# Kernel tuning notes

Measured on AMD Instinct MI355X. Metric: run time of the kernel, lower is better.

## Reference

```python
import jax, jax.numpy as jnp
import numpy as np

DIM_M = 512
NEG_INF = -1e30


def setup_inputs() -> dict:
    key = jax.random.key(0)
    k1, k2, k3, k4, k5, k6, k7 = jax.random.split(key, 7)
    B, Lc, Lq, d = 16, 1024, 512, DIM_M
    C = jax.random.normal(k1, (B, Lc, d), dtype=jnp.float32)
    Q = jax.random.normal(k2, (B, Lq, d), dtype=jnp.float32)
    cmask = jax.random.randint(k3, (B, Lc), 0, 2).astype(jnp.float32)
    qmask = jax.random.randint(k4, (B, Lq), 0, 2).astype(jnp.float32)
    lim = np.sqrt(1.0 / d)
    w = jax.random.uniform(k5, (3 * d,), minval=-lim, maxval=lim, dtype=jnp.float32)
    # out_linear: Linear(4d -> d), torch default init
    bound = np.sqrt(1.0 / (4 * d))
    out_w = jax.random.uniform(k6, (d, 4 * d), minval=-bound, maxval=bound, dtype=jnp.float32)
    out_b = jax.random.uniform(k7, (d,), minval=-bound, maxval=bound, dtype=jnp.float32)
    return {"C": C, "Q": Q, "cmask": cmask, "qmask": qmask, "w": w, "out_w": out_w, "out_b": out_b}


def _mask_logits(t, m):
    return t * m + (1.0 - m) * NEG_INF


def reference(C, Q, cmask, qmask, w, out_w, out_b):
    d = C.shape[-1]
    w1, w2, w3 = w[:d], w[d:2 * d], w[2 * d:]
    # Decomposed trilinear similarity (same math as cat([Ct,Qt,Ct*Qt]) @ w):
    # S[b,i,j] = C[b,i]@w1 + Q[b,j]@w2 + (C[b,i]*w3) @ Q[b,j]
    S = (C @ w1)[:, :, None] + (Q @ w2)[:, None, :] \
        + jnp.einsum('bid,bjd->bij', C * w3, Q)  # [B, Lc, Lq]
    qm = qmask[:, None, :]  # [B, 1, Lq]
    cm = cmask[:, :, None]  # [B, Lc, 1]
    S1 = jax.nn.softmax(_mask_logits(S, qm), axis=2)  # over Lq
    S2 = jax.nn.softmax(_mask_logits(S, cm), axis=1)  # over Lc
    A = jnp.einsum('bij,bjd->bid', S1, Q)  # [B, Lc, d]
    # bmm(bmm(S1, S2^T), C) == S1 @ (S2^T @ C) by associativity (cheaper)
    S2TC = jnp.einsum('bij,bid->bjd', S2, C)  # [B, Lq, d]
    Bm = jnp.einsum('bij,bjd->bid', S1, S2TC)  # [B, Lc, d]
    out = jnp.concatenate([C, A, C * A, C * Bm], axis=2)  # [B, Lc, 4d]
    # dropout inactive (inference); out_linear
    return out @ out_w.T + out_b
```

## Files before the change

### kernel.cpp

```cpp
#include <hip/hip_runtime.h>
#include <hip/hip_bf16.h>


#define NB 16
#define LC 1024
#define LQ 512
#define DM 512
#define D4 2048
#define NEGINF (-1e30f)
#define BK 32
#define LDAp 40

typedef __bf16 v8bf __attribute__((ext_vector_type(8)));
typedef __bf16 v4bf __attribute__((ext_vector_type(4)));
typedef float  v4f  __attribute__((ext_vector_type(4)));

#define MFMA16 __builtin_amdgcn_mfma_f32_16x16x32_bf16

#define TILE_SETUP \
  const int t = threadIdx.x, lane = t & 63, wave = t >> 6; \
  const int wm = wave >> 1, wn = wave & 1, quad = lane >> 4, col = lane & 15;

#define ZERO_ACC \
  v4f acc[4][4]; \
  _Pragma("unroll") for (int x = 0; x < 4; ++x) \
  _Pragma("unroll") for (int y = 0; y < 4; ++y) \
  _Pragma("unroll") for (int r = 0; r < 4; ++r) acc[x][y][r] = 0.f;

#define FRAG_MMA(AL, BL) do { \
  v8bf af_[4], bf_[4]; \
  _Pragma("unroll") for (int x = 0; x < 4; ++x) \
    af_[x] = *(const v8bf*)&AL[(wm * 64 + x * 16 + col) * LDAp + quad * 8]; \
  _Pragma("unroll") for (int y = 0; y < 4; ++y) \
    bf_[y] = *(const v8bf*)&BL[(wn * 64 + y * 16 + col) * LDAp + quad * 8]; \
  _Pragma("unroll") for (int x = 0; x < 4; ++x) \
  _Pragma("unroll") for (int y = 0; y < 4; ++y) \
    acc[x][y] = MFMA16(af_[x], bf_[y], acc[x][y], 0, 0, 0); \
} while (0)

__device__ __forceinline__ void xcd_remap(int& bx, int& by, int& bz) {
  const int gx = gridDim.x, gy = gridDim.y, gz = gridDim.z;
  int flat = bx + gx * (by + gy * bz);
  int per = (gx * gy * gz) >> 3;
  int nw = (flat & 7) * per + (flat >> 3);
  bx = nw % gx;
  int r = nw / gx;
  by = r % gy;
  bz = r / gy;
}

__global__ void k_rowdots(const float* __restrict__ C, const float* __restrict__ Q,
                          const float* __restrict__ w,
                          float* __restrict__ cw1, float* __restrict__ qw2) {
  const int wid = threadIdx.x >> 6, lane = threadIdx.x & 63;
  const int row = blockIdx.x * 4 + wid;
  const bool isC = row < NB * LC;
  const float* src = isC ? (C + (size_t)row * DM) : (Q + (size_t)(row - NB * LC) * DM);
  const float* wv  = isC ? w : (w + DM);
  float v = 0.f;
#pragma unroll
  for (int tt = 0; tt < 8; ++tt) {
    int k = lane + 64 * tt;
    v += src[k] * wv[k];
  }
#pragma unroll
  for (int off = 32; off; off >>= 1) v += __shfl_down(v, off, 64);
  if (lane == 0) {
    if (isC) cw1[row] = v;
    else     qw2[row - NB * LC] = v;
  }
}

__global__ __launch_bounds__(256) void k_mfma_S(
    const float* __restrict__ C, const float* __restrict__ Q, const float* __restrict__ w,
    const float* __restrict__ cw1, const float* __restrict__ qw2, float* __restrict__ S) {
  __shared__ __bf16 Al[128 * LDAp], Bl[128 * LDAp];
  int bx = blockIdx.x, by = blockIdx.y, bz = blockIdx.z;
  xcd_remap(bx, by, bz);
  const int b = bz, i0 = by * 128, j0 = bx * 128;
  TILE_SETUP
  const float* Cb = C + (size_t)b * LC * DM;
  const float* Qb = Q + (size_t)b * LQ * DM;
  const float* w3 = w + 2 * DM;
  const int sr = t >> 1, skc = (t & 1) * 16;
  ZERO_ACC
  for (int k0 = 0; k0 < DM; k0 += BK) {
    const float* ca = Cb + (size_t)(i0 + sr) * DM + k0 + skc;
    const float* qa = Qb + (size_t)(j0 + sr) * DM + k0 + skc;
    const float* wa = w3 + k0 + skc;
#pragma unroll
    for (int u = 0; u < 4; ++u) {
      float4 cf = *(const float4*)(ca + 4 * u);
      float4 wf = *(const float4*)(wa + 4 * u);
      float4 qf = *(const float4*)(qa + 4 * u);
      v4bf ah, bh;
      ah[0] = (__bf16)(cf.x * wf.x); ah[1] = (__bf16)(cf.y * wf.y);
      ah[2] = (__bf16)(cf.z * wf.z); ah[3] = (__bf16)(cf.w * wf.w);
      bh[0] = (__bf16)qf.x; bh[1] = (__bf16)qf.y; bh[2] = (__bf16)qf.z; bh[3] = (__bf16)qf.w;
      *(v4bf*)&Al[sr * LDAp + skc + 4 * u] = ah;
      *(v4bf*)&Bl[sr * LDAp + skc + 4 * u] = bh;
    }
    __syncthreads();
    FRAG_MMA(Al, Bl);
    __syncthreads();
  }
  float* Sb = S + (size_t)b * LC * LQ;
#pragma unroll
  for (int x = 0; x < 4; ++x) {
    const int mB = i0 + wm * 64 + x * 16 + quad * 4;
    float cv[4];
#pragma unroll
    for (int r = 0; r < 4; ++r) cv[r] = cw1[b * LC + mB + r];
#pragma unroll
    for (int y = 0; y < 4; ++y) {
      const int j = j0 + wn * 64 + y * 16 + col;
      const float qv = qw2[b * LQ + j];
#pragma unroll
      for (int r = 0; r < 4; ++r)
        Sb[(size_t)(mB + r) * LQ + j] = acc[x][y][r] + cv[r] + qv;
    }
  }
}

__global__ __launch_bounds__(1024) void k_softstat(
    const float* __restrict__ S, const float* __restrict__ qmask,
    const float* __restrict__ cmask, __bf16* __restrict__ S1,
    float2* __restrict__ pstat) {
  __shared__ float2 cst[16][LQ];
  const int b = blockIdx.y, ic = blockIdx.x;
  const int tid = threadIdx.x, wv = tid >> 6, lane = tid & 63;
  const float* qm  = qmask + b * LQ;
  const float* cm  = cmask + b * LC + ic * 64;
  const float* Sb  = S  + ((size_t)b * LC + ic * 64) * LQ;
  __bf16*      S1b = S1 + ((size_t)b * LC + ic * 64) * LQ;
  float colm[8], cols[8];
#pragma unroll
  for (int tt = 0; tt < 8; ++tt) { colm[tt] = -3e38f; cols[tt] = 0.f; }
  for (int it = 0; it < 4; ++it) {
    const int r = wv * 4 + it;
    const float cmv = cm[r];
    const float* Srow = Sb + (size_t)r * LQ;
    float sv[8], l1[8];
    float m = -3e38f;
#pragma unroll
    for (int tt = 0; tt < 8; ++tt) {
      int j = lane + 64 * tt;
      sv[tt] = Srow[j];
      float qv = qm[j];
      l1[tt] = qv * sv[tt] + (1.f - qv) * NEGINF;
      m = fmaxf(m, l1[tt]);
    }
#pragma unroll
    for (int off = 32; off; off >>= 1) m = fmaxf(m, __shfl_xor(m, off, 64));
    float e[8], s = 0.f;
#pragma unroll
    for (int tt = 0; tt < 8; ++tt) { e[tt] = __expf(l1[tt] - m); s += e[tt]; }
#pragma unroll
    for (int off = 32; off; off >>= 1) s += __shfl_xor(s, off, 64);
    const float inv = 1.f / s;
#pragma unroll
    for (int tt = 0; tt < 8; ++tt)
      S1b[(size_t)r * LQ + lane + 64 * tt] = (__bf16)(e[tt] * inv);
#pragma unroll
    for (int tt = 0; tt < 8; ++tt) {
      float l2 = cmv * sv[tt] + (1.f - cmv) * NEGINF;
      if (l2 > colm[tt]) { cols[tt] *= __expf(colm[tt] - l2); colm[tt] = l2; }
      cols[tt] += __expf(l2 - colm[tt]);
    }
  }
#pragma unroll
  for (int tt = 0; tt < 8; ++tt) cst[wv][lane + 64 * tt] = make_float2(colm[tt], cols[tt]);
  __syncthreads();
  if (tid < LQ) {
    float M = -3e38f, Sd = 0.f;
#pragma unroll
    for (int k = 0; k < 16; ++k) {
      float2 p = cst[k][tid];
      float nM = fmaxf(M, p.x);
      Sd = Sd * __expf(M - nM) + p.y * __expf(p.x - nM);
      M = nM;
    }
    pstat[((size_t)(b * 16 + ic) * LQ) + tid] = make_float2(M, Sd);
  }
}

__global__ void k_colwrite(const float* __restrict__ S, const float* __restrict__ cmask,
                           const float2* __restrict__ pstat, __bf16* __restrict__ S2) {
  __shared__ float Mf[64], If[64];
  const int b = blockIdx.z, ic = blockIdx.y, j0 = blockIdx.x * 64;
  const int c = threadIdx.x & 63, ip = threadIdx.x >> 6;
  if (threadIdx.x < 64) {
    float M = -3e38f, Sd = 0.f;
#pragma unroll
    for (int k = 0; k < 16; ++k) {
      float2 p = pstat[((size_t)(b * 16 + k) * LQ) + j0 + threadIdx.x];
      float nM = fmaxf(M, p.x);
      Sd = Sd * __expf(M - nM) + p.y * __expf(p.x - nM);
      M = nM;
    }
    Mf[threadIdx.x] = M; If[threadIdx.x] = 1.f / Sd;
  }
  __syncthreads();
  const float M = Mf[c], inv = If[c];
  const float* Sb = S + ((size_t)b * LC + ic * 64) * LQ;
  const float* cm = cmask + b * LC + ic * 64;
  __bf16* S2b = S2 + ((size_t)b * LC + ic * 64) * LQ;
  for (int r = ip; r < 64; r += 4) {
    float mk = cm[r];
    float logit = mk * Sb[(size_t)r * LQ + j0 + c] + (1.f - mk) * NEGINF;
    S2b[(size_t)r * LQ + j0 + c] = (__bf16)(__expf(logit - M) * inv);
  }
}

__global__ __launch_bounds__(256) void k_mfma_A(
    const __bf16* __restrict__ S1, const float* __restrict__ Q, __bf16* __restrict__ Aw) {
  __shared__ __bf16 Al[128 * LDAp], Bl[128 * LDAp];
  int bx = blockIdx.x, by = blockIdx.y, bz = blockIdx.z;
  xcd_remap(bx, by, bz);
  const int b = bz, i0 = by * 128, n0 = bx * 128;
  TILE_SETUP
  const __bf16* S1b = S1 + (size_t)b * LC * LQ;
  const float*  Qb  = Q  + (size_t)b * LQ * DM;
  const int ar = t >> 1, akc = (t & 1) * 16;
  const int kk = t >> 3, nn = (t & 7) * 16;
  ZERO_ACC
  for (int k0 = 0; k0 < LQ; k0 += BK) {
    const __bf16* sa = S1b + (size_t)(i0 + ar) * LQ + k0 + akc;
#pragma unroll
    for (int u = 0; u < 2; ++u)
      *(v8bf*)&Al[ar * LDAp + akc + 8 * u] = *(const v8bf*)(sa + 8 * u);
    const float* qa = Qb + (size_t)(k0 + kk) * DM + n0 + nn;
#pragma unroll
    for (int u = 0; u < 4; ++u) {
      float4 f = *(const float4*)(qa + 4 * u);
      Bl[(nn + 4 * u + 0) * LDAp + kk] = (__bf16)f.x;
      Bl[(nn + 4 * u + 1) * LDAp + kk] = (__bf16)f.y;
      Bl[(nn + 4 * u + 2) * LDAp + kk] = (__bf16)f.z;
      Bl[(nn + 4 * u + 3) * LDAp + kk] = (__bf16)f.w;
    }
    __syncthreads();
    FRAG_MMA(Al, Bl);
    __syncthreads();
  }
  __bf16* Ab = Aw + (size_t)b * LC * DM;
#pragma unroll
  for (int x = 0; x < 4; ++x) {
    const int mB = i0 + wm * 64 + x * 16 + quad * 4;
#pragma unroll
    for (int y = 0; y < 4; ++y) {
      const int n = n0 + wn * 64 + y * 16 + col;
#pragma unroll
      for (int r = 0; r < 4; ++r)
        Ab[(size_t)(mB + r) * DM + n] = (__bf16)acc[x][y][r];
    }
  }
}

__global__ __launch_bounds__(256) void k_mfma_T(
    const __bf16* __restrict__ S2, const float* __restrict__ C, __bf16* __restrict__ S2TCT) {
  __shared__ __bf16 Al[128 * LDAp], Bl[128 * LDAp];
  int bx = blockIdx.x, by = blockIdx.y, bz = blockIdx.z;
  xcd_remap(bx, by, bz);
  const int b = bz, j0 = by * 128, n0 = bx * 128;
  TILE_SETUP
  const __bf16* S2b = S2 + (size_t)b * LC * LQ;
  const float*  Cb  = C  + (size_t)b * LC * DM;
  const int kk = t >> 3, jj = (t & 7) * 16;
  ZERO_ACC
  for (int k0 = 0; k0 < LC; k0 += BK) {
    const __bf16* sa = S2b + (size_t)(k0 + kk) * LQ + j0 + jj;
    v8bf s0 = *(const v8bf*)(sa), s1 = *(const v8bf*)(sa + 8);
#pragma unroll
    for (int u = 0; u < 8; ++u) {
      Al[(jj + u) * LDAp + kk]     = s0[u];
      Al[(jj + 8 + u) * LDAp + kk] = s1[u];
    }
    const float* cb2 = Cb + (size_t)(k0 + kk) * DM + n0 + jj;
#pragma unroll
    for (int u = 0; u < 4; ++u) {
      float4 f = *(const float4*)(cb2 + 4 * u);
      Bl[(jj + 4 * u + 0) * LDAp + kk] = (__bf16)f.x;
      Bl[(jj + 4 * u + 1) * LDAp + kk] = (__bf16)f.y;
      Bl[(jj + 4 * u + 2) * LDAp + kk] = (__bf16)f.z;
      Bl[(jj + 4 * u + 3) * LDAp + kk] = (__bf16)f.w;
    }
    __syncthreads();
    FRAG_MMA(Al, Bl);
    __syncthreads();
  }
#pragma unroll
  for (int x = 0; x < 4; ++x) {
    const int jB = j0 + wm * 64 + x * 16 + quad * 4;
#pragma unroll
    for (int y = 0; y < 4; ++y) {
      const int n = n0 + wn * 64 + y * 16 + col;
      v4bf h;
#pragma unroll
      for (int r = 0; r < 4; ++r) h[r] = (__bf16)acc[x][y][r];
      *(v4bf*)&S2TCT[((size_t)b * DM + n) * LQ + jB] = h;
    }
  }
}

__global__ __launch_bounds__(256) void k_mfma_Bm(
    const __bf16* __restrict__ S1, const __bf16* __restrict__ S2TCT, __bf16* __restrict__ Bmw) {
  __shared__ __bf16 Al[128 * LDAp], Bl[128 * LDAp];
  int bx = blockIdx.x, by = blockIdx.y, bz = blockIdx.z;
  xcd_remap(bx, by, bz);
  const int b = bz, i0 = by * 128, n0 = bx * 128;
  TILE_SETUP
  const __bf16* S1b = S1 + (size_t)b * LC * LQ;
  const __bf16* Tb  = S2TCT + (size_t)b * DM * LQ;
  const int ar = t >> 1, akc = (t & 1) * 16;
  ZERO_ACC
  for (int k0 = 0; k0 < LQ; k0 += BK) {
    const __bf16* sa = S1b + (size_t)(i0 + ar) * LQ + k0 + akc;
    const __bf16* ta = Tb + (size_t)(n0 + ar) * LQ + k0 + akc;
#pragma unroll
    for (int u = 0; u < 2; ++u) {
      *(v8bf*)&Al[ar * LDAp + akc + 8 * u] = *(const v8bf*)(sa + 8 * u);
      *(v8bf*)&Bl[ar * LDAp + akc + 8 * u] = *(const v8bf*)(ta + 8 * u);
    }
    __syncthreads();
    FRAG_MMA(Al, Bl);
    __syncthreads();
  }
  __bf16* Bb = Bmw + (size_t)b * LC * DM;
#pragma unroll
  for (int x = 0; x < 4; ++x) {
    const int mB = i0 + wm * 64 + x * 16 + quad * 4;
#pragma unroll
    for (int y = 0; y < 4; ++y) {
      const int n = n0 + wn * 64 + y * 16 + col;
#pragma unroll
      for (int r = 0; r < 4; ++r)
        Bb[(size_t)(mB + r) * DM + n] = (__bf16)acc[x][y][r];
    }
  }
}

__global__ __launch_bounds__(256) void k_mfma_out(
    const float* __restrict__ C, const __bf16* __restrict__ Aw, const __bf16* __restrict__ Bmw,
    const float* __restrict__ OW, const float* __restrict__ ob, float* __restrict__ out) {
  __shared__ __bf16 Asg[4][128 * LDAp], Bsg[4][128 * LDAp];
  int bx = blockIdx.x, by = blockIdx.y, bz = blockIdx.z;
  xcd_remap(bx, by, bz);
  const int b = bz, i0 = by * 128, n0 = bx * 128;
  TILE_SETUP
  const float*  Cb = C   + (size_t)b * LC * DM;
  const __bf16* Ab = Aw  + (size_t)b * LC * DM;
  const __bf16* Bb = Bmw + (size_t)b * LC * DM;
  const int sr = t >> 1, skc = (t & 1) * 16;
  ZERO_ACC
  for (int kl0 = 0; kl0 < DM; kl0 += BK) {
    const float*  cr = Cb + (size_t)(i0 + sr) * DM + kl0 + skc;
    const __bf16* ap = Ab + (size_t)(i0 + sr) * DM + kl0 + skc;
    const __bf16* bp = Bb + (size_t)(i0 + sr) * DM + kl0 + skc;
#pragma unroll
    for (int u = 0; u < 2; ++u) {
      float4 f0 = *(const float4*)(cr + 8 * u);
      float4 f1 = *(const float4*)(cr + 8 * u + 4);
      v8bf av = *(const v8bf*)(ap + 8 * u);
      v8bf bv = *(const v8bf*)(bp + 8 * u);
      float cf[8] = {f0.x, f0.y, f0.z, f0.w, f1.x, f1.y, f1.z, f1.w};
      v8bf hC, hCA, hCB;
#pragma unroll
      for (int e = 0; e < 8; ++e) {
        hC[e]  = (__bf16)cf[e];
        hCA[e] = (__bf16)(cf[e] * (float)av[e]);
        hCB[e] = (__bf16)(cf[e] * (float)bv[e]);
      }
      const int off = sr * LDAp + skc + 8 * u;
      *(v8bf*)&Asg[0][off] = hC;
      *(v8bf*)&Asg[1][off] = av;
      *(v8bf*)&Asg[2][off] = hCA;
      *(v8bf*)&Asg[3][off] = hCB;
    }
    const float* owr = OW + (size_t)(n0 + sr) * D4 + kl0 + skc;
#pragma unroll
    for (int s = 0; s < 4; ++s) {
#pragma unroll
      for (int u = 0; u < 4; ++u) {
        float4 f = *(const float4*)(owr + s * DM + 4 * u);
        v4bf h; h[0] = (__bf16)f.x; h[1] = (__bf16)f.y; h[2] = (__bf16)f.z; h[3] = (__bf16)f.w;
        *(v4bf*)&Bsg[s][sr * LDAp + skc + 4 * u] = h;
      }
    }
    __syncthreads();
#pragma unroll
    for (int s = 0; s < 4; ++s) FRAG_MMA(Asg[s], Bsg[s]);
    __syncthreads();
  }
  float* outb = out + (size_t)b * LC * DM;
#pragma unroll
  for (int x = 0; x < 4; ++x) {
    const int mB = i0 + wm * 64 + x * 16 + quad * 4;
#pragma unroll
    for (int y = 0; y < 4; ++y) {
      const int n = n0 + wn * 64 + y * 16 + col;
      const float bv = ob[n];
#pragma unroll
      for (int r = 0; r < 4; ++r)
        outb[(size_t)(mB + r) * DM + n] = acc[x][y][r] + bv;
    }
  }
}

extern "C" void kernel_launch(void* const* d_in, const int* in_sizes, int n_in,
                              void* d_out, int out_size, void* d_ws, size_t ws_size,
                              hipStream_t stream) {
  const float* C     = (const float*)d_in[0];
  const float* Q     = (const float*)d_in[1];
  const float* cmask = (const float*)d_in[2];
  const float* qmask = (const float*)d_in[3];
  const float* w     = (const float*)d_in[4];
  const float* out_w = (const float*)d_in[5];
  const float* out_b = (const float*)d_in[6];
  float* out = (float*)d_out;

  char* base = (char*)d_ws;
  float*  cw1   = (float*)base;
  float*  qw2   = (float*)(base + 65536);
  char*   R     = base + 131072;
  float*  S     = (float*)R;
  __bf16* Aw    = (__bf16*)R;
  __bf16* Bmw   = (__bf16*)(R + (16u << 20));
  __bf16* S1    = (__bf16*)(base + 131072 + (32u << 20));
  __bf16* S2    = (__bf16*)(base + 131072 + (48u << 20));
  __bf16* S2TCT = (__bf16*)(base + 131072 + (64u << 20));
  float2* pstat = (float2*)S2TCT;
  (void)in_sizes; (void)n_in; (void)out_size; (void)ws_size;

  k_rowdots<<<(NB * LC + NB * LQ) / 4, 256, 0, stream>>>(C, Q, w, cw1, qw2);
  k_mfma_S<<<dim3(LQ / 128, LC / 128, NB), 256, 0, stream>>>(C, Q, w, cw1, qw2, S);
  k_softstat<<<dim3(LC / 64, NB), 1024, 0, stream>>>(S, qmask, cmask, S1, pstat);
  k_colwrite<<<dim3(LQ / 64, LC / 64, NB), 256, 0, stream>>>(S, cmask, pstat, S2);
  k_mfma_A<<<dim3(DM / 128, LC / 128, NB), 256, 0, stream>>>(S1, Q, Aw);
  k_mfma_T<<<dim3(DM / 128, LQ / 128, NB), 256, 0, stream>>>(S2, C, S2TCT);
  k_mfma_Bm<<<dim3(DM / 128, LC / 128, NB), 256, 0, stream>>>(S1, S2TCT, Bmw);
  k_mfma_out<<<dim3(DM / 128, LC / 128, NB), 256, 0, stream>>>(C, Aw, Bmw, out_w, out_b, out);
}
```

Baseline: 319.3 us.

## Pre-transpose Q, C and S2 to bf16 and use 8-wave GEMM tiles

Adds a transpose kernel that writes bf16 transposed copies of Q and C, and makes the column-softmax kernel emit S2 transposed through an LDS tile. With these layouts the A and T GEMMs can fill LDS with contiguous vector loads instead of scattered scalar transposed stores. All MFMA kernels move to 512-thread blocks, 8 waves with a 64x32 tile per wave, and the output GEMM runs in two passes over half-size LDS buffers. The cost is two extra transpose launches and more workspace traffic, with buffers aliased in the workspace.

```diff
diff --git a/kernel.cpp b/kernel.cpp
--- a/kernel.cpp
+++ b/kernel.cpp
@@ -17,24 +17,25 @@
 
 #define MFMA16 __builtin_amdgcn_mfma_f32_16x16x32_bf16
 
-#define TILE_SETUP \
+#define TILE_SETUP8 \
   const int t = threadIdx.x, lane = t & 63, wave = t >> 6; \
-  const int wm = wave >> 1, wn = wave & 1, quad = lane >> 4, col = lane & 15;
-
-#define ZERO_ACC \
-  v4f acc[4][4]; \
+  const int wm = wave >> 2, wn = wave & 3, quad = lane >> 4, col = lane & 15; \
+  const int sr = t >> 2, skc = (t & 3) * 8;
+
+#define ZERO_ACC8 \
+  v4f acc[4][2]; \
   _Pragma("unroll") for (int x = 0; x < 4; ++x) \
-  _Pragma("unroll") for (int y = 0; y < 4; ++y) \
+  _Pragma("unroll") for (int y = 0; y < 2; ++y) \
   _Pragma("unroll") for (int r = 0; r < 4; ++r) acc[x][y][r] = 0.f;
 
-#define FRAG_MMA(AL, BL) do { \
-  v8bf af_[4], bf_[4]; \
+#define FRAG_MMA8(AL, BL) do { \
+  v8bf af_[4], bf_[2]; \
   _Pragma("unroll") for (int x = 0; x < 4; ++x) \
     af_[x] = *(const v8bf*)&AL[(wm * 64 + x * 16 + col) * LDAp + quad * 8]; \
-  _Pragma("unroll") for (int y = 0; y < 4; ++y) \
-    bf_[y] = *(const v8bf*)&BL[(wn * 64 + y * 16 + col) * LDAp + quad * 8]; \
+  _Pragma("unroll") for (int y = 0; y < 2; ++y) \
+    bf_[y] = *(const v8bf*)&BL[(wn * 32 + y * 16 + col) * LDAp + quad * 8]; \
   _Pragma("unroll") for (int x = 0; x < 4; ++x) \
-  _Pragma("unroll") for (int y = 0; y < 4; ++y) \
+  _Pragma("unroll") for (int y = 0; y < 2; ++y) \
     acc[x][y] = MFMA16(af_[x], bf_[y], acc[x][y], 0, 0, 0); \
 } while (0)
 
@@ -49,6 +50,14 @@
   bz = r / gy;
 }
 
+__device__ __forceinline__ v8bf cvt8(const float* p) {
+  float4 f0 = *(const float4*)p, f1 = *(const float4*)(p + 4);
+  v8bf h;
+  h[0] = (__bf16)f0.x; h[1] = (__bf16)f0.y; h[2] = (__bf16)f0.z; h[3] = (__bf16)f0.w;
+  h[4] = (__bf16)f1.x; h[5] = (__bf16)f1.y; h[6] = (__bf16)f1.z; h[7] = (__bf16)f1.w;
+  return h;
+}
+
 __global__ void k_rowdots(const float* __restrict__ C, const float* __restrict__ Q,
                           const float* __restrict__ w,
                           float* __restrict__ cw1, float* __restrict__ qw2) {
@@ -71,37 +80,48 @@
   }
 }
 
-__global__ __launch_bounds__(256) void k_mfma_S(
+__global__ void k_transpose(const float* __restrict__ in, __bf16* __restrict__ outT,
+                            int R, int Cd) {
+  __shared__ __bf16 tile[64][66];
+  const int b = blockIdx.z;
+  const int r0 = blockIdx.y * 64, c0 = blockIdx.x * 64;
+  const int tr = threadIdx.x >> 6, tc = threadIdx.x & 63;
+  const float* inb = in + (size_t)b * R * Cd;
+  __bf16* outb = outT + (size_t)b * Cd * R;
+  for (int r = tr; r < 64; r += 4)
+    tile[r][tc] = (__bf16)inb[(size_t)(r0 + r) * Cd + c0 + tc];
+  __syncthreads();
+  for (int c = tr; c < 64; c += 4)
+    outb[(size_t)(c0 + c) * R + r0 + tc] = tile[tc][c];
+}
+
+__global__ __launch_bounds__(512) void k_mfma_S(
     const float* __restrict__ C, const float* __restrict__ Q, const float* __restrict__ w,
     const float* __restrict__ cw1, const float* __restrict__ qw2, float* __restrict__ S) {
   __shared__ __bf16 Al[128 * LDAp], Bl[128 * LDAp];
   int bx = blockIdx.x, by = blockIdx.y, bz = blockIdx.z;
   xcd_remap(bx, by, bz);
   const int b = bz, i0 = by * 128, j0 = bx * 128;
-  TILE_SETUP
+  TILE_SETUP8
   const float* Cb = C + (size_t)b * LC * DM;
   const float* Qb = Q + (size_t)b * LQ * DM;
   const float* w3 = w + 2 * DM;
-  const int sr = t >> 1, skc = (t & 1) * 16;
-  ZERO_ACC
+  ZERO_ACC8
   for (int k0 = 0; k0 < DM; k0 += BK) {
     const float* ca = Cb + (size_t)(i0 + sr) * DM + k0 + skc;
     const float* qa = Qb + (size_t)(j0 + sr) * DM + k0 + skc;
     const float* wa = w3 + k0 + skc;
-#pragma unroll
-    for (int u = 0; u < 4; ++u) {
-      float4 cf = *(const float4*)(ca + 4 * u);
-      float4 wf = *(const float4*)(wa + 4 * u);
-      float4 qf = *(const float4*)(qa + 4 * u);
-      v4bf ah, bh;
-      ah[0] = (__bf16)(cf.x * wf.x); ah[1] = (__bf16)(cf.y * wf.y);
-      ah[2] = (__bf16)(cf.z * wf.z); ah[3] = (__bf16)(cf.w * wf.w);
-      bh[0] = (__bf16)qf.x; bh[1] = (__bf16)qf.y; bh[2] = (__bf16)qf.z; bh[3] = (__bf16)qf.w;
-      *(v4bf*)&Al[sr * LDAp + skc + 4 * u] = ah;
-      *(v4bf*)&Bl[sr * LDAp + skc + 4 * u] = bh;
-    }
-    __syncthreads();
-    FRAG_MMA(Al, Bl);
+    float4 c0 = *(const float4*)ca, c1 = *(const float4*)(ca + 4);
+    float4 w0 = *(const float4*)wa, w1 = *(const float4*)(wa + 4);
+    v8bf ah;
+    ah[0] = (__bf16)(c0.x * w0.x); ah[1] = (__bf16)(c0.y * w0.y);
+    ah[2] = (__bf16)(c0.z * w0.z); ah[3] = (__bf16)(c0.w * w0.w);
+    ah[4] = (__bf16)(c1.x * w1.x); ah[5] = (__bf16)(c1.y * w1.y);
+    ah[6] = (__bf16)(c1.z * w1.z); ah[7] = (__bf16)(c1.w * w1.w);
+    *(v8bf*)&Al[sr * LDAp + skc] = ah;
+    *(v8bf*)&Bl[sr * LDAp + skc] = cvt8(qa);
+    __syncthreads();
+    FRAG_MMA8(Al, Bl);
     __syncthreads();
   }
   float* Sb = S + (size_t)b * LC * LQ;
@@ -112,8 +132,8 @@
 #pragma unroll
     for (int r = 0; r < 4; ++r) cv[r] = cw1[b * LC + mB + r];
 #pragma unroll
-    for (int y = 0; y < 4; ++y) {
-      const int j = j0 + wn * 64 + y * 16 + col;
+    for (int y = 0; y < 2; ++y) {
+      const int j = j0 + wn * 32 + y * 16 + col;
       const float qv = qw2[b * LQ + j];
 #pragma unroll
       for (int r = 0; r < 4; ++r)
@@ -185,8 +205,9 @@
 }
 
 __global__ void k_colwrite(const float* __restrict__ S, const float* __restrict__ cmask,
-                           const float2* __restrict__ pstat, __bf16* __restrict__ S2) {
+                           const float2* __restrict__ pstat, __bf16* __restrict__ S2T) {
   __shared__ float Mf[64], If[64];
+  __shared__ __bf16 tile[64][66];
   const int b = blockIdx.z, ic = blockIdx.y, j0 = blockIdx.x * 64;
   const int c = threadIdx.x & 63, ip = threadIdx.x >> 6;
   if (threadIdx.x < 64) {
@@ -204,42 +225,32 @@
   const float M = Mf[c], inv = If[c];
   const float* Sb = S + ((size_t)b * LC + ic * 64) * LQ;
   const float* cm = cmask + b * LC + ic * 64;
-  __bf16* S2b = S2 + ((size_t)b * LC + ic * 64) * LQ;
   for (int r = ip; r < 64; r += 4) {
     float mk = cm[r];
     float logit = mk * Sb[(size_t)r * LQ + j0 + c] + (1.f - mk) * NEGINF;
-    S2b[(size_t)r * LQ + j0 + c] = (__bf16)(__expf(logit - M) * inv);
-  }
-}
-
-__global__ __launch_bounds__(256) void k_mfma_A(
-    const __bf16* __restrict__ S1, const float* __restrict__ Q, __bf16* __restrict__ Aw) {
+    tile[r][c] = (__bf16)(__expf(logit - M) * inv);
+  }
+  __syncthreads();
+  __bf16* S2Tb = S2T + ((size_t)b * LQ + j0) * LC + ic * 64;
+  for (int jr = ip; jr < 64; jr += 4)
+    S2Tb[(size_t)jr * LC + c] = tile[c][jr];
+}
+
+__global__ __launch_bounds__(512) void k_mfma_A(
+    const __bf16* __restrict__ S1, const __bf16* __restrict__ QT, __bf16* __restrict__ Aw) {
   __shared__ __bf16 Al[128 * LDAp], Bl[128 * LDAp];
   int bx = blockIdx.x, by = blockIdx.y, bz = blockIdx.z;
   xcd_remap(bx, by, bz);
   const int b = bz, i0 = by * 128, n0 = bx * 128;
-  TILE_SETUP
+  TILE_SETUP8
   const __bf16* S1b = S1 + (size_t)b * LC * LQ;
-  const float*  Qb  = Q  + (size_t)b * LQ * DM;
-  const int ar = t >> 1, akc = (t & 1) * 16;
-  const int kk = t >> 3, nn = (t & 7) * 16;
-  ZERO_ACC
+  const __bf16* QTb = QT + (size_t)b * DM * LQ;
+  ZERO_ACC8
   for (int k0 = 0; k0 < LQ; k0 += BK) {
-    const __bf16* sa = S1b + (size_t)(i0 + ar) * LQ + k0 + akc;
-#pragma unroll
-    for (int u = 0; u < 2; ++u)
-      *(v8bf*)&Al[ar * LDAp + akc + 8 * u] = *(const v8bf*)(sa + 8 * u);
-    const float* qa = Qb + (size_t)(k0 + kk) * DM + n0 + nn;
-#pragma unroll
-    for (int u = 0; u < 4; ++u) {
-      float4 f = *(const float4*)(qa + 4 * u);
-      Bl[(nn + 4 * u + 0) * LDAp + kk] = (__bf16)f.x;
-      Bl[(nn + 4 * u + 1) * LDAp + kk] = (__bf16)f.y;
-      Bl[(nn + 4 * u + 2) * LDAp + kk] = (__bf16)f.z;
-      Bl[(nn + 4 * u + 3) * LDAp + kk] = (__bf16)f.w;
-    }
-    __syncthreads();
-    FRAG_MMA(Al, Bl);
+    *(v8bf*)&Al[sr * LDAp + skc] = *(const v8bf*)(S1b + (size_t)(i0 + sr) * LQ + k0 + skc);
+    *(v8bf*)&Bl[sr * LDAp + skc] = *(const v8bf*)(QTb + (size_t)(n0 + sr) * LQ + k0 + skc);
+    __syncthreads();
+    FRAG_MMA8(Al, Bl);
     __syncthreads();
   }
   __bf16* Ab = Aw + (size_t)b * LC * DM;
@@ -247,8 +258,8 @@
   for (int x = 0; x < 4; ++x) {
     const int mB = i0 + wm * 64 + x * 16 + quad * 4;
 #pragma unroll
-    for (int y = 0; y < 4; ++y) {
-      const int n = n0 + wn * 64 + y * 16 + col;
+    for (int y = 0; y < 2; ++y) {
+      const int n = n0 + wn * 32 + y * 16 + col;
 #pragma unroll
       for (int r = 0; r < 4; ++r)
         Ab[(size_t)(mB + r) * DM + n] = (__bf16)acc[x][y][r];
@@ -256,44 +267,29 @@
   }
 }
 
-__global__ __launch_bounds__(256) void k_mfma_T(
-    const __bf16* __restrict__ S2, const float* __restrict__ C, __bf16* __restrict__ S2TCT) {
+__global__ __launch_bounds__(512) void k_mfma_T(
+    const __bf16* __restrict__ S2T, const __bf16* __restrict__ CT, __bf16* __restrict__ S2TCT) {
   __shared__ __bf16 Al[128 * LDAp], Bl[128 * LDAp];
   int bx = blockIdx.x, by = blockIdx.y, bz = blockIdx.z;
   xcd_remap(bx, by, bz);
   const int b = bz, j0 = by * 128, n0 = bx * 128;
-  TILE_SETUP
-  const __bf16* S2b = S2 + (size_t)b * LC * LQ;
-  const float*  Cb  = C  + (size_t)b * LC * DM;
-  const int kk = t >> 3, jj = (t & 7) * 16;
-  ZERO_ACC
+  TILE_SETUP8
+  const __bf16* S2Tb = S2T + (size_t)b * LQ * LC;
+  const __bf16* CTb  = CT  + (size_t)b * DM * LC;
+  ZERO_ACC8
   for (int k0 = 0; k0 < LC; k0 += BK) {
-    const __bf16* sa = S2b + (size_t)(k0 + kk) * LQ + j0 + jj;
-    v8bf s0 = *(const v8bf*)(sa), s1 = *(const v8bf*)(sa + 8);
-#pragma unroll
-    for (int u = 0; u < 8; ++u) {
-      Al[(jj + u) * LDAp + kk]     = s0[u];
-      Al[(jj + 8 + u) * LDAp + kk] = s1[u];
-    }
-    const float* cb2 = Cb + (size_t)(k0 + kk) * DM + n0 + jj;
-#pragma unroll
-    for (int u = 0; u < 4; ++u) {
-      float4 f = *(const float4*)(cb2 + 4 * u);
-      Bl[(jj + 4 * u + 0) * LDAp + kk] = (__bf16)f.x;
-      Bl[(jj + 4 * u + 1) * LDAp + kk] = (__bf16)f.y;
-      Bl[(jj + 4 * u + 2) * LDAp + kk] = (__bf16)f.z;
-      Bl[(jj + 4 * u + 3) * LDAp + kk] = (__bf16)f.w;
-    }
-    __syncthreads();
-    FRAG_MMA(Al, Bl);
+    *(v8bf*)&Al[sr * LDAp + skc] = *(const v8bf*)(S2Tb + (size_t)(j0 + sr) * LC + k0 + skc);
+    *(v8bf*)&Bl[sr * LDAp + skc] = *(const v8bf*)(CTb  + (size_t)(n0 + sr) * LC + k0 + skc);
+    __syncthreads();
+    FRAG_MMA8(Al, Bl);
     __syncthreads();
   }
 #pragma unroll
   for (int x = 0; x < 4; ++x) {
     const int jB = j0 + wm * 64 + x * 16 + quad * 4;
 #pragma unroll
-    for (int y = 0; y < 4; ++y) {
-      const int n = n0 + wn * 64 + y * 16 + col;
+    for (int y = 0; y < 2; ++y) {
+      const int n = n0 + wn * 32 + y * 16 + col;
       v4bf h;
 #pragma unroll
       for (int r = 0; r < 4; ++r) h[r] = (__bf16)acc[x][y][r];
@@ -302,27 +298,21 @@
   }
 }
 
-__global__ __launch_bounds__(256) void k_mfma_Bm(
+__global__ __launch_bounds__(512) void k_mfma_Bm(
     const __bf16* __restrict__ S1, const __bf16* __restrict__ S2TCT, __bf16* __restrict__ Bmw) {
   __shared__ __bf16 Al[128 * LDAp], Bl[128 * LDAp];
   int bx = blockIdx.x, by = blockIdx.y, bz = blockIdx.z;
   xcd_remap(bx, by, bz);
   const int b = bz, i0 = by * 128, n0 = bx * 128;
-  TILE_SETUP
+  TILE_SETUP8
   const __bf16* S1b = S1 + (size_t)b * LC * LQ;
   const __bf16* Tb  = S2TCT + (size_t)b * DM * LQ;
-  const int ar = t >> 1, akc = (t & 1) * 16;
-  ZERO_ACC
+  ZERO_ACC8
   for (int k0 = 0; k0 < LQ; k0 += BK) {
-    const __bf16* sa = S1b + (size_t)(i0 + ar) * LQ + k0 + akc;
-    const __bf16* ta = Tb + (size_t)(n0 + ar) * LQ + k0 + akc;
-#pragma unroll
-    for (int u = 0; u < 2; ++u) {
-      *(v8bf*)&Al[ar * LDAp + akc + 8 * u] = *(const v8bf*)(sa + 8 * u);
-      *(v8bf*)&Bl[ar * LDAp + akc + 8 * u] = *(const v8bf*)(ta + 8 * u);
-    }
-    __syncthreads();
-    FRAG_MMA(Al, Bl);
+    *(v8bf*)&Al[sr * LDAp + skc] = *(const v8bf*)(S1b + (size_t)(i0 + sr) * LQ + k0 + skc);
+    *(v8bf*)&Bl[sr * LDAp + skc] = *(const v8bf*)(Tb  + (size_t)(n0 + sr) * LQ + k0 + skc);
+    __syncthreads();
+    FRAG_MMA8(Al, Bl);
     __syncthreads();
   }
   __bf16* Bb = Bmw + (size_t)b * LC * DM;
@@ -330,8 +320,8 @@
   for (int x = 0; x < 4; ++x) {
     const int mB = i0 + wm * 64 + x * 16 + quad * 4;
 #pragma unroll
-    for (int y = 0; y < 4; ++y) {
-      const int n = n0 + wn * 64 + y * 16 + col;
+    for (int y = 0; y < 2; ++y) {
+      const int n = n0 + wn * 32 + y * 16 + col;
 #pragma unroll
       for (int r = 0; r < 4; ++r)
         Bb[(size_t)(mB + r) * DM + n] = (__bf16)acc[x][y][r];
@@ -339,65 +329,57 @@
   }
 }
 
-__global__ __launch_bounds__(256) void k_mfma_out(
+__global__ __launch_bounds__(512) void k_mfma_out(
     const float* __restrict__ C, const __bf16* __restrict__ Aw, const __bf16* __restrict__ Bmw,
     const float* __restrict__ OW, const float* __restrict__ ob, float* __restrict__ out) {
-  __shared__ __bf16 Asg[4][128 * LDAp], Bsg[4][128 * LDAp];
+  __shared__ __bf16 Asg[2][128 * LDAp], Bsg[2][128 * LDAp];
   int bx = blockIdx.x, by = blockIdx.y, bz = blockIdx.z;
   xcd_remap(bx, by, bz);
   const int b = bz, i0 = by * 128, n0 = bx * 128;
-  TILE_SETUP
+  TILE_SETUP8
   const float*  Cb = C   + (size_t)b * LC * DM;
   const __bf16* Ab = Aw  + (size_t)b * LC * DM;
   const __bf16* Bb = Bmw + (size_t)b * LC * DM;
-  const int sr = t >> 1, skc = (t & 1) * 16;
-  ZERO_ACC
-  for (int kl0 = 0; kl0 < DM; kl0 += BK) {
-    const float*  cr = Cb + (size_t)(i0 + sr) * DM + kl0 + skc;
-    const __bf16* ap = Ab + (size_t)(i0 + sr) * DM + kl0 + skc;
-    const __bf16* bp = Bb + (size_t)(i0 + sr) * DM + kl0 + skc;
-#pragma unroll
-    for (int u = 0; u < 2; ++u) {
-      float4 f0 = *(const float4*)(cr + 8 * u);
-      float4 f1 = *(const float4*)(cr + 8 * u + 4);
-      v8bf av = *(const v8bf*)(ap + 8 * u);
-      v8bf bv = *(const v8bf*)(bp + 8 * u);
-      float cf[8] = {f0.x, f0.y, f0.z, f0.w, f1.x, f1.y, f1.z, f1.w};
-      v8bf hC, hCA, hCB;
-#pragma unroll
-      for (int e = 0; e < 8; ++e) {
-        hC[e]  = (__bf16)cf[e];
-        hCA[e] = (__bf16)(cf[e] * (float)av[e]);
-        hCB[e] = (__bf16)(cf[e] * (float)bv[e]);
+  ZERO_ACC8
+#pragma unroll
+  for (int pass = 0; pass < 2; ++pass) {
+    for (int kl0 = 0; kl0 < DM; kl0 += BK) {
+      const float*  cr = Cb + (size_t)(i0 + sr) * DM + kl0 + skc;
+      const __bf16* ap = Ab + (size_t)(i0 + sr) * DM + kl0 + skc;
+      const int off = sr * LDAp + skc;
+      v8bf av = *(const v8bf*)ap;
+      if (pass == 0) {
+        *(v8bf*)&Asg[0][off] = cvt8(cr);
+        *(v8bf*)&Asg[1][off] = av;
+      } else {
+        float4 f0 = *(const float4*)cr, f1 = *(const float4*)(cr + 4);
+        v8bf bv = *(const v8bf*)(Bb + (size_t)(i0 + sr) * DM + kl0 + skc);
+        float cf[8] = {f0.x, f0.y, f0.z, f0.w, f1.x, f1.y, f1.z, f1.w};
+        v8bf hCA, hCB;
+#pragma unroll
+        for (int e = 0; e < 8; ++e) {
+          hCA[e] = (__bf16)(cf[e] * (float)av[e]);
+          hCB[e] = (__bf16)(cf[e] * (float)bv[e]);
+        }
+        *(v8bf*)&Asg[0][off] = hCA;
+        *(v8bf*)&Asg[1][off] = hCB;
       }
-      const int off = sr * LDAp + skc + 8 * u;
-      *(v8bf*)&Asg[0][off] = hC;
-      *(v8bf*)&Asg[1][off] = av;
-      *(v8bf*)&Asg[2][off] = hCA;
-      *(v8bf*)&Asg[3][off] = hCB;
-    }
-    const float* owr = OW + (size_t)(n0 + sr) * D4 + kl0 + skc;
-#pragma unroll
-    for (int s = 0; s < 4; ++s) {
-#pragma unroll
-      for (int u = 0; u < 4; ++u) {
-        float4 f = *(const float4*)(owr + s * DM + 4 * u);
-        v4bf h; h[0] = (__bf16)f.x; h[1] = (__bf16)f.y; h[2] = (__bf16)f.z; h[3] = (__bf16)f.w;
-        *(v4bf*)&Bsg[s][sr * LDAp + skc + 4 * u] = h;
-      }
-    }
-    __syncthreads();
-#pragma unroll
-    for (int s = 0; s < 4; ++s) FRAG_MMA(Asg[s], Bsg[s]);
-    __syncthreads();
+      const float* owr = OW + (size_t)(n0 + sr) * D4 + pass * 2 * DM + kl0 + skc;
+      *(v8bf*)&Bsg[0][off] = cvt8(owr);
+      *(v8bf*)&Bsg[1][off] = cvt8(owr + DM);
+      __syncthreads();
+      FRAG_MMA8(Asg[0], Bsg[0]);
+      FRAG_MMA8(Asg[1], Bsg[1]);
+      __syncthreads();
+    }
   }
   float* outb = out + (size_t)b * LC * DM;
 #pragma unroll
   for (int x = 0; x < 4; ++x) {
     const int mB = i0 + wm * 64 + x * 16 + quad * 4;
 #pragma unroll
-    for (int y = 0; y < 4; ++y) {
-      const int n = n0 + wn * 64 + y * 16 + col;
+    for (int y = 0; y < 2; ++y) {
+      const int n = n0 + wn * 32 + y * 16 + col;
       const float bv = ob[n];
 #pragma unroll
       for (int r = 0; r < 4; ++r)
@@ -424,19 +406,24 @@
   char*   R     = base + 131072;
   float*  S     = (float*)R;
   __bf16* Aw    = (__bf16*)R;
+  __bf16* CT    = (__bf16*)(R + (16u << 20));
   __bf16* Bmw   = (__bf16*)(R + (16u << 20));
   __bf16* S1    = (__bf16*)(base + 131072 + (32u << 20));
-  __bf16* S2    = (__bf16*)(base + 131072 + (48u << 20));
-  __bf16* S2TCT = (__bf16*)(base + 131072 + (64u << 20));
-  float2* pstat = (float2*)S2TCT;
+  __bf16* S2T   = (__bf16*)(base + 131072 + (48u << 20));
+  char*   Z     = base + 131072 + (64u << 20);
+  float2* pstat = (float2*)Z;
+  __bf16* QT    = (__bf16*)Z;
+  __bf16* S2TCT = (__bf16*)Z;
   (void)in_sizes; (void)n_in; (void)out_size; (void)ws_size;
 
   k_rowdots<<<(NB * LC + NB * LQ) / 4, 256, 0, stream>>>(C, Q, w, cw1, qw2);
-  k_mfma_S<<<dim3(LQ / 128, LC / 128, NB), 256, 0, stream>>>(C, Q, w, cw1, qw2, S);
+  k_mfma_S<<<dim3(LQ / 128, LC / 128, NB), 512, 0, stream>>>(C, Q, w, cw1, qw2, S);
   k_softstat<<<dim3(LC / 64, NB), 1024, 0, stream>>>(S, qmask, cmask, S1, pstat);
-  k_colwrite<<<dim3(LQ / 64, LC / 64, NB), 256, 0, stream>>>(S, cmask, pstat, S2);
-  k_mfma_A<<<dim3(DM / 128, LC / 128, NB), 256, 0, stream>>>(S1, Q, Aw);
-  k_mfma_T<<<dim3(DM / 128, LQ / 128, NB), 256, 0, stream>>>(S2, C, S2TCT);
-  k_mfma_Bm<<<dim3(DM / 128, LC / 128, NB), 256, 0, stream>>>(S1, S2TCT, Bmw);
-  k_mfma_out<<<dim3(DM / 128, LC / 128, NB), 256, 0, stream>>>(C, Aw, Bmw, out_w, out_b, out);
-}
+  k_colwrite<<<dim3(LQ / 64, LC / 64, NB), 256, 0, stream>>>(S, cmask, pstat, S2T);
+  k_transpose<<<dim3(DM / 64, LQ / 64, NB), 256, 0, stream>>>(Q, QT, LQ, DM);
+  k_transpose<<<dim3(DM / 64, LC / 64, NB), 256, 0, stream>>>(C, CT, LC, DM);
+  k_mfma_A<<<dim3(DM / 128, LC / 128, NB), 512, 0, stream>>>(S1, QT, Aw);
+  k_mfma_T<<<dim3(DM / 128, LQ / 128, NB), 512, 0, stream>>>(S2T, CT, S2TCT);
+  k_mfma_Bm<<<dim3(DM / 128, LC / 128, NB), 512, 0, stream>>>(S1, S2TCT, Bmw);
+  k_mfma_out<<<dim3(DM / 128, LC / 128, NB), 512, 0, stream>>>(C, Aw, Bmw, out_w, out_b, out);
+}
```

Measured after the change: 299.1 us. -6.4%, faster.
